# Performance work log

Hardware: AMD Instinct MI355X
Metric: run time of the kernel (lower is better)

The kernel has to match this reference:

```python
import jax, jax.numpy as jnp
import numpy as np

N = 8192
IN_DIM = 1024
HID = 64
N_CLASS = 40
N_LAYERS = 4  # N_LAYERS-1 hidden GraphConvolutions + 1 output layer


def _row_normalize(a):
    return a / jnp.clip(a.sum(axis=1, keepdims=True), 1e-6)


def setup_inputs() -> dict:
    key = jax.random.key(0)
    ks = jax.random.split(key, 10)
    x = jax.random.normal(ks[0], (N, IN_DIM), dtype=jnp.float32)
    # symmetric-ish normalized dense adjacency surrogates
    adj1 = _row_normalize(jax.random.uniform(ks[1], (N, N), dtype=jnp.float32))
    adj2 = _row_normalize(jax.random.uniform(ks[2], (N, N), dtype=jnp.float32))
    s_in = 1.0 / np.sqrt(IN_DIM)
    s_h = 1.0 / np.sqrt(HID)
    fc1_W = jax.random.uniform(ks[3], (IN_DIM, HID), minval=-s_in, maxval=s_in)
    fc1_b = jnp.zeros((HID,), jnp.float32)
    W_h = jax.random.uniform(ks[4], (N_LAYERS - 1, HID, HID), minval=-s_h, maxval=s_h)
    b_h = jnp.zeros((N_LAYERS - 1, HID), jnp.float32)
    W_out = jax.random.uniform(ks[5], (HID, N_CLASS), minval=-s_h, maxval=s_h)
    b_out = jnp.zeros((N_CLASS,), jnp.float32)
    return {"x": x, "adj1": adj1, "adj2": adj2, "fc1_W": fc1_W, "fc1_b": fc1_b,
            "W_h": W_h, "b_h": b_h, "W_out": W_out, "b_out": b_out}


def reference(x, adj1, adj2, fc1_W, fc1_b, W_h, b_h, W_out, b_out):
    # fc1 projection (dropout is identity in eval mode)
    h = x @ fc1_W + fc1_b  # [N, HID]
    # hidden GraphConvolution layers: aggregate, bias, residual, relu
    for i in range(W_h.shape[0]):
        h = jax.nn.relu(adj1 @ (h @ W_h[i]) + b_h[i] + h)
    # final layer: no residual
    out = jax.nn.relu(adj1 @ (h @ W_out) + b_out)  # [N, N_CLASS]
    return out
```

## Files before the change

kernel.cpp:

```cpp
#include <hip/hip_runtime.h>
#include <hip/hip_bf16.h>

typedef __attribute__((ext_vector_type(8))) short short8;
typedef __attribute__((ext_vector_type(4))) float f32x4;
typedef __attribute__((ext_vector_type(4))) int i32x4;

#define NROWS 8192
#define MTILE 128
#define SK 8
#define SA 400000.0f
#define SB 15.875f
#define INVQ (1.0f / (SA * SB))

__device__ inline short f2bf(float f) {
  union { float f; unsigned u; } v; v.f = f;
  unsigned r = v.u + 0x7FFFu + ((v.u >> 16) & 1u);
  return (short)(r >> 16);
}

__global__ __launch_bounds__(256) void prep_kernel(
    const float* __restrict__ x, const float* __restrict__ Wfc,
    float* __restrict__ P,
    const float* __restrict__ adj, char* __restrict__ AQ) {
  int bid = blockIdx.x;
  if (!AQ || bid < 1024) {
    __shared__ short Ws[64][136];
    int tid = threadIdx.x;
    int mb = bid & 127, yb = bid >> 7;
    int k0 = yb * 128;
    for (int i = tid; i < 2048; i += 256) {
      int k = i >> 4, nq = (i & 15) << 2;
      f32x4 v = *(const f32x4*)(Wfc + (size_t)(k0 + k) * 64 + nq);
      Ws[nq][k] = f2bf(v.x); Ws[nq + 1][k] = f2bf(v.y);
      Ws[nq + 2][k] = f2bf(v.z); Ws[nq + 3][k] = f2bf(v.w);
    }
    __syncthreads();
    int w = tid >> 6;
    int l = tid & 63;
    int l15 = l & 15, kg = l >> 4;
    int m_base = mb * 64 + w * 16;
    const float* Arow = x + (size_t)(m_base + l15) * 1024 + k0;
    f32x4 acc[4] = {{0,0,0,0},{0,0,0,0},{0,0,0,0},{0,0,0,0}};
#pragma unroll
    for (int k = 0; k < 128; k += 64) {
      f32x4 a32[2][2];
      short8 b[2][4];
#pragma unroll
      for (int u = 0; u < 2; ++u) {
        int kk = k + u * 32 + kg * 8;
        a32[u][0] = *(const f32x4*)(Arow + kk);
        a32[u][1] = *(const f32x4*)(Arow + kk + 4);
        b[u][0] = *(const short8*)&Ws[l15 +  0][kk];
        b[u][1] = *(const short8*)&Ws[l15 + 16][kk];
        b[u][2] = *(const short8*)&Ws[l15 + 32][kk];
        b[u][3] = *(const short8*)&Ws[l15 + 48][kk];
      }
#pragma unroll
      for (int u = 0; u < 2; ++u) {
        short8 af;
        af[0] = f2bf(a32[u][0].x); af[1] = f2bf(a32[u][0].y);
        af[2] = f2bf(a32[u][0].z); af[3] = f2bf(a32[u][0].w);
        af[4] = f2bf(a32[u][1].x); af[5] = f2bf(a32[u][1].y);
        af[6] = f2bf(a32[u][1].z); af[7] = f2bf(a32[u][1].w);
#pragma unroll
        for (int t = 0; t < 4; ++t)
          acc[t] = __builtin_amdgcn_mfma_f32_16x16x32_bf16(af, b[u][t], acc[t], 0, 0, 0);
      }
    }
    float* Pb = P + (size_t)yb * (NROWS * 64);
    int mr = m_base + kg * 4;
#pragma unroll
    for (int r = 0; r < 4; ++r) {
      size_t base = (size_t)(mr + r) * 64 + l15;
#pragma unroll
      for (int t = 0; t < 4; ++t) Pb[base + 16 * t] = acc[t][r];
    }
  } else {
    const size_t total = (size_t)NROWS * NROWS;
    size_t i0 = ((size_t)(bid - 1024) * 256 + threadIdx.x) * 16;
    size_t stride = (size_t)2048 * 256 * 16;
    for (size_t i = i0; i < total; i += stride) {
      i32x4 o;
#pragma unroll
      for (int q = 0; q < 4; ++q) {
        f32x4 v = __builtin_nontemporal_load((const f32x4*)(adj + i + 4 * q));
        int r0 = (int)(v.x * SA + 0.5f); r0 = r0 > 127 ? 127 : r0;
        int r1 = (int)(v.y * SA + 0.5f); r1 = r1 > 127 ? 127 : r1;
        int r2 = (int)(v.z * SA + 0.5f); r2 = r2 > 127 ? 127 : r2;
        int r3 = (int)(v.w * SA + 0.5f); r3 = r3 > 127 ? 127 : r3;
        o[q] = (r0 & 255) | ((r1 & 255) << 8) | ((r2 & 255) << 16) | ((r3 & 255) << 24);
      }
      *(i32x4*)(AQ + i) = o;
    }
  }
}

__global__ __launch_bounds__(256, 2) void gemm_i8_kernel(
    const char* __restrict__ AQ, const char* __restrict__ BQ,
    int* __restrict__ P) {
  __shared__ __align__(16) char Bs[64][1024 + 16];
  int tid = threadIdx.x;
  int w = tid >> 6, l = tid & 63;
  int l15 = l & 15, kg = l >> 4;
  int wrow = blockIdx.x * MTILE + w * 32;
  const int KCH = NROWS / SK;
  int k0 = blockIdx.y * KCH;
  const char* A0 = AQ + (size_t)(wrow + l15) * NROWS + k0;
  const char* A1 = AQ + (size_t)(wrow + 16 + l15) * NROWS + k0;

#pragma unroll
  for (int j = 0; j < 16; ++j) {
    int slot = tid + 256 * j;
    int r = slot >> 6, c = (slot & 63) << 4;
    i32x4 v = *(const i32x4*)(BQ + (size_t)r * NROWS + k0 + c);
    *(i32x4*)&Bs[r][c] = v;
  }
  __syncthreads();

  i32x4 acc[2][4];
#pragma unroll
  for (int rt = 0; rt < 2; ++rt)
#pragma unroll
    for (int ct = 0; ct < 4; ++ct) acc[rt][ct] = (i32x4){0, 0, 0, 0};

#pragma unroll 4
  for (int k = 0; k < KCH; k += 64) {
    int kk = k + kg * 16;
    i32x4 a0 = *(const i32x4*)(A0 + kk);
    i32x4 a1 = *(const i32x4*)(A1 + kk);
    i32x4 b0 = *(const i32x4*)&Bs[l15 +  0][kk];
    i32x4 b1 = *(const i32x4*)&Bs[l15 + 16][kk];
    i32x4 b2 = *(const i32x4*)&Bs[l15 + 32][kk];
    i32x4 b3 = *(const i32x4*)&Bs[l15 + 48][kk];
    acc[0][0] = __builtin_amdgcn_mfma_i32_16x16x64_i8(a0, b0, acc[0][0], 0, 0, 0);
    acc[0][1] = __builtin_amdgcn_mfma_i32_16x16x64_i8(a0, b1, acc[0][1], 0, 0, 0);
    acc[0][2] = __builtin_amdgcn_mfma_i32_16x16x64_i8(a0, b2, acc[0][2], 0, 0, 0);
    acc[0][3] = __builtin_amdgcn_mfma_i32_16x16x64_i8(a0, b3, acc[0][3], 0, 0, 0);
    acc[1][0] = __builtin_amdgcn_mfma_i32_16x16x64_i8(a1, b0, acc[1][0], 0, 0, 0);
    acc[1][1] = __builtin_amdgcn_mfma_i32_16x16x64_i8(a1, b1, acc[1][1], 0, 0, 0);
    acc[1][2] = __builtin_amdgcn_mfma_i32_16x16x64_i8(a1, b2, acc[1][2], 0, 0, 0);
    acc[1][3] = __builtin_amdgcn_mfma_i32_16x16x64_i8(a1, b3, acc[1][3], 0, 0, 0);
  }

  int* Pb = P + (size_t)blockIdx.y * (NROWS * 64);
#pragma unroll
  for (int rt = 0; rt < 2; ++rt)
#pragma unroll
    for (int r = 0; r < 4; ++r) {
      size_t base = (size_t)(wrow + rt * 16 + kg * 4 + r) * 64 + l15;
#pragma unroll
      for (int ct = 0; ct < 4; ++ct) Pb[base + 16 * ct] = acc[rt][ct][r];
    }
}

__global__ __launch_bounds__(256) void fused_rs_kernel(
    const float* __restrict__ Pf, const int* __restrict__ Pi,
    const float* __restrict__ bias, const float* __restrict__ Hres,
    const float* __restrict__ Wmat, int Nout,
    float* __restrict__ Hout, char* __restrict__ tQ, short* __restrict__ tB,
    int useint, int dores, int wantq) {
  __shared__ float hs[64][68];
  __shared__ float Ws[64][64];
  int tid = threadIdx.x;
  for (int i = tid; i < 64 * 64; i += 256) {
    int j = i >> 6, n = i & 63;
    Ws[j][n] = (n < Nout) ? Wmat[j * Nout + n] : 0.0f;
  }
  int r = tid >> 2;
  int c0 = (tid & 3) << 4;
  size_t gbase = ((size_t)blockIdx.x * 64 + r) * 64 + c0;
  f32x4 s[4] = {{0,0,0,0},{0,0,0,0},{0,0,0,0},{0,0,0,0}};
  if (useint) {
    i32x4 si[4] = {{0,0,0,0},{0,0,0,0},{0,0,0,0},{0,0,0,0}};
    for (int sidx = 0; sidx < SK; ++sidx) {
      const int* Pp = Pi + (size_t)sidx * ((size_t)NROWS * 64) + gbase;
#pragma unroll
      for (int q = 0; q < 4; ++q) si[q] += *(const i32x4*)(Pp + 4 * q);
    }
#pragma unroll
    for (int q = 0; q < 4; ++q) s[q] = __builtin_convertvector(si[q], f32x4) * INVQ;
  } else {
    for (int sidx = 0; sidx < SK; ++sidx) {
      const float* Pp = Pf + (size_t)sidx * ((size_t)NROWS * 64) + gbase;
#pragma unroll
      for (int q = 0; q < 4; ++q) s[q] += *(const f32x4*)(Pp + 4 * q);
    }
  }
#pragma unroll
  for (int q = 0; q < 4; ++q) {
    f32x4 v = s[q] + *(const f32x4*)(bias + c0 + 4 * q);
    if (dores) {
      v += *(const f32x4*)(Hres + gbase + 4 * q);
      v.x = v.x > 0.f ? v.x : 0.f; v.y = v.y > 0.f ? v.y : 0.f;
      v.z = v.z > 0.f ? v.z : 0.f; v.w = v.w > 0.f ? v.w : 0.f;
    }
    *(f32x4*)(Hout + gbase + 4 * q) = v;
    *(f32x4*)&hs[r][c0 + 4 * q] = v;
  }
  __syncthreads();
  int m = tid >> 2;
  int nq = (tid & 3) << 4;
  float hr[64];
#pragma unroll
  for (int j = 0; j < 64; j += 4) {
    f32x4 v = *(const f32x4*)&hs[m][j];
    hr[j] = v.x; hr[j + 1] = v.y; hr[j + 2] = v.z; hr[j + 3] = v.w;
  }
  size_t mglob = (size_t)blockIdx.x * 64 + m;
#pragma unroll
  for (int ni = 0; ni < 16; ++ni) {
    int n = nq + ni;
    float acc = 0.0f;
#pragma unroll
    for (int j = 0; j < 64; ++j) acc += hr[j] * Ws[j][n];
    if (wantq) {
      int q = __float2int_rn(acc * SB);
      q = q > 127 ? 127 : (q < -127 ? -127 : q);
      tQ[(size_t)n * NROWS + mglob] = (char)q;
    } else {
      tB[(size_t)n * NROWS + mglob] = f2bf(acc);
    }
  }
}

__global__ __launch_bounds__(256, 2) void gemm_a32_u2(
    const float* __restrict__ A, const short* __restrict__ BT,
    float* __restrict__ P, int K) {
  int w = threadIdx.x >> 6;
  int l = threadIdx.x & 63;
  int l15 = l & 15, kg = l >> 4;
  int m_base = blockIdx.x * 64 + w * 16;
  const float* Arow = A + (size_t)(m_base + l15) * K;
  const short* Br = BT + (size_t)l15 * K;
  int kchunk = K / SK;
  int k0 = blockIdx.y * kchunk;
  f32x4 acc[4] = {{0,0,0,0},{0,0,0,0},{0,0,0,0},{0,0,0,0}};
  for (int k = k0; k < k0 + kchunk; k += 64) {
    f32x4 a32[2][2];
    short8 b[2][4];
#pragma unroll
    for (int u = 0; u < 2; ++u) {
      int kk = k + u * 32 + kg * 8;
      a32[u][0] = __builtin_nontemporal_load((const f32x4*)(Arow + kk));
      a32[u][1] = __builtin_nontemporal_load((const f32x4*)(Arow + kk + 4));
      b[u][0] = *(const short8*)(Br + kk);
      b[u][1] = *(const short8*)(Br + (size_t)16 * K + kk);
      b[u][2] = *(const short8*)(Br + (size_t)32 * K + kk);
      b[u][3] = *(const short8*)(Br + (size_t)48 * K + kk);
    }
#pragma unroll
    for (int u = 0; u < 2; ++u) {
      short8 af;
      af[0] = f2bf(a32[u][0].x); af[1] = f2bf(a32[u][0].y);
      af[2] = f2bf(a32[u][0].z); af[3] = f2bf(a32[u][0].w);
      af[4] = f2bf(a32[u][1].x); af[5] = f2bf(a32[u][1].y);
      af[6] = f2bf(a32[u][1].z); af[7] = f2bf(a32[u][1].w);
#pragma unroll
      for (int t = 0; t < 4; ++t)
        acc[t] = __builtin_amdgcn_mfma_f32_16x16x32_bf16(af, b[u][t], acc[t], 0, 0, 0);
    }
  }
  float* Pb = P + (size_t)blockIdx.y * (NROWS * 64);
  int mr = m_base + kg * 4;
#pragma unroll
  for (int r = 0; r < 4; ++r) {
    size_t base = (size_t)(mr + r) * 64 + l15;
#pragma unroll
    for (int t = 0; t < 4; ++t) Pb[base + 16 * t] = acc[t][r];
  }
}

__global__ __launch_bounds__(256) void reduce_out_kernel(
    const float* __restrict__ Pf, const int* __restrict__ Pi,
    const float* __restrict__ bias, float* __restrict__ Out, int useint) {
  int gid = blockIdx.x * 256 + threadIdx.x;
  int e0 = gid * 4;
  int n = e0 & 63;
  if (n >= 40) return;
  f32x4 s = {0, 0, 0, 0};
  if (useint) {
    i32x4 si = {0, 0, 0, 0};
    for (int sidx = 0; sidx < SK; ++sidx)
      si += *(const i32x4*)(Pi + (size_t)sidx * (NROWS * 64) + e0);
    s = __builtin_convertvector(si, f32x4) * INVQ;
  } else {
    for (int sidx = 0; sidx < SK; ++sidx)
      s += *(const f32x4*)(Pf + (size_t)sidx * (NROWS * 64) + e0);
  }
  s += *(const f32x4*)(bias + n);
  s.x = s.x > 0.f ? s.x : 0.f; s.y = s.y > 0.f ? s.y : 0.f;
  s.z = s.z > 0.f ? s.z : 0.f; s.w = s.w > 0.f ? s.w : 0.f;
  int m = e0 >> 6;
  *(f32x4*)(Out + (size_t)m * 40 + n) = s;
}

extern "C" void kernel_launch(void* const* d_in, const int* in_sizes, int n_in,
                              void* d_out, int out_size, void* d_ws, size_t ws_size,
                              hipStream_t stream) {
  const float* x     = (const float*)d_in[0];
  const float* adj1  = (const float*)d_in[1];
  const float* fc1_W = (const float*)d_in[3];
  const float* fc1_b = (const float*)d_in[4];
  const float* W_h   = (const float*)d_in[5];
  const float* b_h   = (const float*)d_in[6];
  const float* W_out = (const float*)d_in[7];
  const float* b_out = (const float*)d_in[8];
  float* out = (float*)d_out;

  char* ws = (char*)d_ws;
  size_t off = 0;
  float* P    = (float*)(ws + off); off += (size_t)SK * NROWS * 64 * 4;
  int*   Pi   = (int*)P;
  float* h_a  = (float*)(ws + off); off += (size_t)NROWS * 64 * 4;
  float* h_b  = (float*)(ws + off); off += (size_t)NROWS * 64 * 4;
  short* tB   = (short*)(ws + off); off += (size_t)64 * NROWS * 2;
  char*  tQ   = (char*)(ws + off);  off += (size_t)64 * NROWS;
  size_t aq_bytes = (size_t)NROWS * NROWS;
  char*  AQ   = (ws_size - off >= aq_bytes) ? (char*)(ws + off) : nullptr;
  int ok = AQ != nullptr;

  prep_kernel<<<ok ? 3072 : 1024, 256, 0, stream>>>(x, fc1_W, P, adj1, AQ);

  fused_rs_kernel<<<NROWS / 64, 256, 0, stream>>>(
      P, nullptr, fc1_b, nullptr, W_h, 64, h_a, tQ, tB, 0, 0, ok);

  float* hc = h_a; float* hn = h_b;
  for (int i = 0; i < 3; ++i) {
    if (ok)
      gemm_i8_kernel<<<dim3(NROWS / MTILE, SK), 256, 0, stream>>>(AQ, tQ, Pi);
    else
      gemm_a32_u2<<<dim3(NROWS / 64, SK), 256, 0, stream>>>(adj1, tB, P, NROWS);
    const float* Wn = (i < 2) ? (W_h + (size_t)(i + 1) * 64 * 64) : W_out;
    int Nn = (i < 2) ? 64 : 40;
    fused_rs_kernel<<<NROWS / 64, 256, 0, stream>>>(
        P, Pi, b_h + (size_t)i * 64, hc, Wn, Nn, hn, tQ, tB, ok, 1, ok);
    float* t = hc; hc = hn; hn = t;
  }

  if (ok)
    gemm_i8_kernel<<<dim3(NROWS / MTILE, SK), 256, 0, stream>>>(AQ, tQ, Pi);
  else
    gemm_a32_u2<<<dim3(NROWS / 64, SK), 256, 0, stream>>>(adj1, tB, P, NROWS);
  reduce_out_kernel<<<NROWS * 64 / 4 / 256, 256, 0, stream>>>(P, Pi, b_out, out, ok);
}
```

Before: 233.5 us.

## Fuse split-K reduction and next-layer projection into GEMM via last-block atomic counter

Each split-K GEMM block now bumps a per-row-tile atomic counter after writing its partials. The last block to finish reduces all partials, applies bias, residual and relu, and computes the next layer's projection into a ping-ponged int8 buffer. This removes the separate fused_rs and reduce_out kernel launches and their dependent round trips. In exchange it adds threadfences, an atomic and a memset, and the reduction runs serially in only one of the SK blocks per tile, which may leave the tail of the grid underused.

```diff
diff --git a/kernel.cpp b/kernel.cpp
--- a/kernel.cpp
+++ b/kernel.cpp
@@ -18,14 +18,23 @@
   return (short)(r >> 16);
 }
 
+__device__ inline float relu4x(float a) { return a > 0.f ? a : 0.f; }
+
 __global__ __launch_bounds__(256) void prep_kernel(
     const float* __restrict__ x, const float* __restrict__ Wfc,
-    float* __restrict__ P,
+    const float* __restrict__ fc1_b, const float* __restrict__ W0,
+    float* __restrict__ P, float* __restrict__ h0,
+    char* __restrict__ tQ, short* __restrict__ tB, int wantq,
+    unsigned* __restrict__ cnt,
     const float* __restrict__ adj, char* __restrict__ AQ) {
   int bid = blockIdx.x;
+  int tid = threadIdx.x;
   if (!AQ || bid < 1024) {
-    __shared__ short Ws[64][136];
-    int tid = threadIdx.x;
+    __shared__ __align__(16) char smem[17408 + 16384];
+    short (*Ws)[136] = (short(*)[136])smem;
+    float (*hs)[68]  = (float(*)[68])smem;
+    float (*Wf)[64]  = (float(*)[64])(smem + 17408);
+    __shared__ unsigned isred;
     int mb = bid & 127, yb = bid >> 7;
     int k0 = yb * 128;
     for (int i = tid; i < 2048; i += 256) {
@@ -35,8 +44,7 @@
       Ws[nq + 2][k] = f2bf(v.z); Ws[nq + 3][k] = f2bf(v.w);
     }
     __syncthreads();
-    int w = tid >> 6;
-    int l = tid & 63;
+    int w = tid >> 6, l = tid & 63;
     int l15 = l & 15, kg = l >> 4;
     int m_base = mb * 64 + w * 16;
     const float* Arow = x + (size_t)(m_base + l15) * 1024 + k0;
@@ -67,7 +75,7 @@
           acc[t] = __builtin_amdgcn_mfma_f32_16x16x32_bf16(af, b[u][t], acc[t], 0, 0, 0);
       }
     }
-    float* Pb = P + (size_t)yb * (NROWS * 64);
+    float* Pb = P + (size_t)yb * ((size_t)NROWS * 64);
     int mr = m_base + kg * 4;
 #pragma unroll
     for (int r = 0; r < 4; ++r) {
@@ -75,9 +83,53 @@
 #pragma unroll
       for (int t = 0; t < 4; ++t) Pb[base + 16 * t] = acc[t][r];
     }
+    __threadfence();
+    __syncthreads();
+    if (tid == 0) isred = (atomicAdd(&cnt[mb], 1u) == SK - 1) ? 1u : 0u;
+    __syncthreads();
+    if (!isred) return;
+    __threadfence();
+    for (int i = tid; i < 4096; i += 256) Wf[i >> 6][i & 63] = W0[i];
+    int r = tid >> 2, c0 = (tid & 3) << 4;
+    size_t gbase = ((size_t)mb * 64 + r) * 64 + c0;
+    f32x4 s[4] = {{0,0,0,0},{0,0,0,0},{0,0,0,0},{0,0,0,0}};
+    for (int sidx = 0; sidx < SK; ++sidx) {
+      const float* Pp = P + (size_t)sidx * ((size_t)NROWS * 64) + gbase;
+#pragma unroll
+      for (int q = 0; q < 4; ++q) s[q] += *(const f32x4*)(Pp + 4 * q);
+    }
+#pragma unroll
+    for (int q = 0; q < 4; ++q) {
+      f32x4 v = s[q] + *(const f32x4*)(fc1_b + c0 + 4 * q);
+      *(f32x4*)(h0 + gbase + 4 * q) = v;
+      *(f32x4*)&hs[r][c0 + 4 * q] = v;
+    }
+    __syncthreads();
+    int m = tid >> 2, nq = (tid & 3) << 4;
+    float hr[64];
+#pragma unroll
+    for (int j = 0; j < 64; j += 4) {
+      f32x4 v = *(const f32x4*)&hs[m][j];
+      hr[j] = v.x; hr[j + 1] = v.y; hr[j + 2] = v.z; hr[j + 3] = v.w;
+    }
+    size_t mglob = (size_t)mb * 64 + m;
+#pragma unroll
+    for (int ni = 0; ni < 16; ++ni) {
+      int n = nq + ni;
+      float a2 = 0.f;
+#pragma unroll
+      for (int j = 0; j < 64; ++j) a2 += hr[j] * Wf[j][n];
+      if (wantq) {
+        int q = __float2int_rn(a2 * SB);
+        q = q > 127 ? 127 : (q < -127 ? -127 : q);
+        tQ[(size_t)n * NROWS + mglob] = (char)q;
+      } else {
+        tB[(size_t)n * NROWS + mglob] = f2bf(a2);
+      }
+    }
   } else {
     const size_t total = (size_t)NROWS * NROWS;
-    size_t i0 = ((size_t)(bid - 1024) * 256 + threadIdx.x) * 16;
+    size_t i0 = ((size_t)(bid - 1024) * 256 + tid) * 16;
     size_t stride = (size_t)2048 * 256 * 16;
     for (size_t i = i0; i < total; i += stride) {
       i32x4 o;
@@ -95,14 +147,20 @@
   }
 }
 
-__global__ __launch_bounds__(256, 2) void gemm_i8_kernel(
+__global__ __launch_bounds__(256, 2) void gemm_i8f_kernel(
     const char* __restrict__ AQ, const char* __restrict__ BQ,
-    int* __restrict__ P) {
+    int* __restrict__ P, unsigned* __restrict__ cnt,
+    const float* __restrict__ bias, const float* __restrict__ Hres,
+    const float* __restrict__ Wnext, int Nout,
+    float* __restrict__ Hout, char* __restrict__ tQn,
+    float* __restrict__ Out, int mode) {
   __shared__ __align__(16) char Bs[64][1024 + 16];
+  __shared__ unsigned isred;
   int tid = threadIdx.x;
   int w = tid >> 6, l = tid & 63;
   int l15 = l & 15, kg = l >> 4;
-  int wrow = blockIdx.x * MTILE + w * 32;
+  int mb = blockIdx.x;
+  int wrow = mb * MTILE + w * 32;
   const int KCH = NROWS / SK;
   int k0 = blockIdx.y * KCH;
   const char* A0 = AQ + (size_t)(wrow + l15) * NROWS + k0;
@@ -112,8 +170,7 @@
   for (int j = 0; j < 16; ++j) {
     int slot = tid + 256 * j;
     int r = slot >> 6, c = (slot & 63) << 4;
-    i32x4 v = *(const i32x4*)(BQ + (size_t)r * NROWS + k0 + c);
-    *(i32x4*)&Bs[r][c] = v;
+    *(i32x4*)&Bs[r][c] = *(const i32x4*)(BQ + (size_t)r * NROWS + k0 + c);
   }
   __syncthreads();
 
@@ -142,7 +199,7 @@
     acc[1][3] = __builtin_amdgcn_mfma_i32_16x16x64_i8(a1, b3, acc[1][3], 0, 0, 0);
   }
 
-  int* Pb = P + (size_t)blockIdx.y * (NROWS * 64);
+  int* Pb = P + (size_t)blockIdx.y * ((size_t)NROWS * 64);
 #pragma unroll
   for (int rt = 0; rt < 2; ++rt)
 #pragma unroll
@@ -151,75 +208,71 @@
 #pragma unroll
       for (int ct = 0; ct < 4; ++ct) Pb[base + 16 * ct] = acc[rt][ct][r];
     }
-}
-
-__global__ __launch_bounds__(256) void fused_rs_kernel(
-    const float* __restrict__ Pf, const int* __restrict__ Pi,
-    const float* __restrict__ bias, const float* __restrict__ Hres,
-    const float* __restrict__ Wmat, int Nout,
-    float* __restrict__ Hout, char* __restrict__ tQ, short* __restrict__ tB,
-    int useint, int dores, int wantq) {
-  __shared__ float hs[64][68];
-  __shared__ float Ws[64][64];
-  int tid = threadIdx.x;
-  for (int i = tid; i < 64 * 64; i += 256) {
-    int j = i >> 6, n = i & 63;
-    Ws[j][n] = (n < Nout) ? Wmat[j * Nout + n] : 0.0f;
-  }
-  int r = tid >> 2;
-  int c0 = (tid & 3) << 4;
-  size_t gbase = ((size_t)blockIdx.x * 64 + r) * 64 + c0;
-  f32x4 s[4] = {{0,0,0,0},{0,0,0,0},{0,0,0,0},{0,0,0,0}};
-  if (useint) {
+
+  __threadfence();
+  __syncthreads();
+  if (tid == 0) isred = (atomicAdd(&cnt[mb], 1u) == SK - 1) ? 1u : 0u;
+  __syncthreads();
+  if (!isred) return;
+  __threadfence();
+
+  float (*hs)[68] = (float(*)[68])&Bs[0][0];
+  float (*Wf)[64] = (float(*)[64])((char*)&Bs[0][0] + 17408);
+  if (mode == 0) {
+    for (int i = tid; i < 4096; i += 256) {
+      int j = i >> 6, n = i & 63;
+      Wf[j][n] = (n < Nout) ? Wnext[j * Nout + n] : 0.0f;
+    }
+  }
+  for (int half = 0; half < 2; ++half) {
+    int row0 = mb * MTILE + half * 64;
+    int r = tid >> 2, c0 = (tid & 3) << 4;
+    size_t gbase = ((size_t)row0 + r) * 64 + c0;
     i32x4 si[4] = {{0,0,0,0},{0,0,0,0},{0,0,0,0},{0,0,0,0}};
     for (int sidx = 0; sidx < SK; ++sidx) {
-      const int* Pp = Pi + (size_t)sidx * ((size_t)NROWS * 64) + gbase;
+      const int* Pp = P + (size_t)sidx * ((size_t)NROWS * 64) + gbase;
 #pragma unroll
       for (int q = 0; q < 4; ++q) si[q] += *(const i32x4*)(Pp + 4 * q);
     }
 #pragma unroll
-    for (int q = 0; q < 4; ++q) s[q] = __builtin_convertvector(si[q], f32x4) * INVQ;
-  } else {
-    for (int sidx = 0; sidx < SK; ++sidx) {
-      const float* Pp = Pf + (size_t)sidx * ((size_t)NROWS * 64) + gbase;
-#pragma unroll
-      for (int q = 0; q < 4; ++q) s[q] += *(const f32x4*)(Pp + 4 * q);
-    }
-  }
-#pragma unroll
-  for (int q = 0; q < 4; ++q) {
-    f32x4 v = s[q] + *(const f32x4*)(bias + c0 + 4 * q);
-    if (dores) {
-      v += *(const f32x4*)(Hres + gbase + 4 * q);
-      v.x = v.x > 0.f ? v.x : 0.f; v.y = v.y > 0.f ? v.y : 0.f;
-      v.z = v.z > 0.f ? v.z : 0.f; v.w = v.w > 0.f ? v.w : 0.f;
-    }
-    *(f32x4*)(Hout + gbase + 4 * q) = v;
-    *(f32x4*)&hs[r][c0 + 4 * q] = v;
-  }
-  __syncthreads();
-  int m = tid >> 2;
-  int nq = (tid & 3) << 4;
-  float hr[64];
-#pragma unroll
-  for (int j = 0; j < 64; j += 4) {
-    f32x4 v = *(const f32x4*)&hs[m][j];
-    hr[j] = v.x; hr[j + 1] = v.y; hr[j + 2] = v.z; hr[j + 3] = v.w;
-  }
-  size_t mglob = (size_t)blockIdx.x * 64 + m;
-#pragma unroll
-  for (int ni = 0; ni < 16; ++ni) {
-    int n = nq + ni;
-    float acc = 0.0f;
-#pragma unroll
-    for (int j = 0; j < 64; ++j) acc += hr[j] * Ws[j][n];
-    if (wantq) {
-      int q = __float2int_rn(acc * SB);
-      q = q > 127 ? 127 : (q < -127 ? -127 : q);
-      tQ[(size_t)n * NROWS + mglob] = (char)q;
-    } else {
-      tB[(size_t)n * NROWS + mglob] = f2bf(acc);
-    }
+    for (int q = 0; q < 4; ++q) {
+      f32x4 v = __builtin_convertvector(si[q], f32x4) * INVQ;
+      v += *(const f32x4*)(bias + c0 + 4 * q);
+      if (mode == 0) {
+        v += *(const f32x4*)(Hres + gbase + 4 * q);
+        v.x = relu4x(v.x); v.y = relu4x(v.y); v.z = relu4x(v.z); v.w = relu4x(v.w);
+        *(f32x4*)(Hout + gbase + 4 * q) = v;
+        *(f32x4*)&hs[r][c0 + 4 * q] = v;
+      } else {
+#pragma unroll
+        for (int e = 0; e < 4; ++e) {
+          int n = c0 + 4 * q + e;
+          if (n < 40) Out[((size_t)row0 + r) * 40 + n] = relu4x(v[e]);
+        }
+      }
+    }
+    __syncthreads();
+    if (mode == 0) {
+      int m = tid >> 2, nq = (tid & 3) << 4;
+      float hr[64];
+#pragma unroll
+      for (int j = 0; j < 64; j += 4) {
+        f32x4 v = *(const f32x4*)&hs[m][j];
+        hr[j] = v.x; hr[j + 1] = v.y; hr[j + 2] = v.z; hr[j + 3] = v.w;
+      }
+      size_t mglob = (size_t)row0 + m;
+#pragma unroll
+      for (int ni = 0; ni < 16; ++ni) {
+        int n = nq + ni;
+        float a2 = 0.f;
+#pragma unroll
+        for (int j = 0; j < 64; ++j) a2 += hr[j] * Wf[j][n];
+        int q = __float2int_rn(a2 * SB);
+        q = q > 127 ? 127 : (q < -127 ? -127 : q);
+        tQn[(size_t)n * NROWS + mglob] = (char)q;
+      }
+    }
+    __syncthreads();
   }
 }
 
@@ -270,26 +323,69 @@
   }
 }
 
+__global__ __launch_bounds__(256) void fused_rs_kernel(
+    const float* __restrict__ Pf,
+    const float* __restrict__ bias, const float* __restrict__ Hres,
+    const float* __restrict__ Wmat, int Nout,
+    float* __restrict__ Hout, short* __restrict__ tB, int dores) {
+  __shared__ float hs[64][68];
+  __shared__ float Ws[64][64];
+  int tid = threadIdx.x;
+  for (int i = tid; i < 64 * 64; i += 256) {
+    int j = i >> 6, n = i & 63;
+    Ws[j][n] = (n < Nout) ? Wmat[j * Nout + n] : 0.0f;
+  }
+  int r = tid >> 2;
+  int c0 = (tid & 3) << 4;
+  size_t gbase = ((size_t)blockIdx.x * 64 + r) * 64 + c0;
+  f32x4 s[4] = {{0,0,0,0},{0,0,0,0},{0,0,0,0},{0,0,0,0}};
+  for (int sidx = 0; sidx < SK; ++sidx) {
+    const float* Pp = Pf + (size_t)sidx * ((size_t)NROWS * 64) + gbase;
+#pragma unroll
+    for (int q = 0; q < 4; ++q) s[q] += *(const f32x4*)(Pp + 4 * q);
+  }
+#pragma unroll
+  for (int q = 0; q < 4; ++q) {
+    f32x4 v = s[q] + *(const f32x4*)(bias + c0 + 4 * q);
+    if (dores) {
+      v += *(const f32x4*)(Hres + gbase + 4 * q);
+      v.x = relu4x(v.x); v.y = relu4x(v.y); v.z = relu4x(v.z); v.w = relu4x(v.w);
+    }
+    *(f32x4*)(Hout + gbase + 4 * q) = v;
+    *(f32x4*)&hs[r][c0 + 4 * q] = v;
+  }
+  __syncthreads();
+  int m = tid >> 2;
+  int nq = (tid & 3) << 4;
+  float hr[64];
+#pragma unroll
+  for (int j = 0; j < 64; j += 4) {
+    f32x4 v = *(const f32x4*)&hs[m][j];
+    hr[j] = v.x; hr[j + 1] = v.y; hr[j + 2] = v.z; hr[j + 3] = v.w;
+  }
+  size_t mglob = (size_t)blockIdx.x * 64 + m;
+#pragma unroll
+  for (int ni = 0; ni < 16; ++ni) {
+    int n = nq + ni;
+    float a2 = 0.0f;
+#pragma unroll
+    for (int j = 0; j < 64; ++j) a2 += hr[j] * Ws[j][n];
+    tB[(size_t)n * NROWS + mglob] = f2bf(a2);
+  }
+}
+
 __global__ __launch_bounds__(256) void reduce_out_kernel(
-    const float* __restrict__ Pf, const int* __restrict__ Pi,
-    const float* __restrict__ bias, float* __restrict__ Out, int useint) {
+    const float* __restrict__ Pf, const float* __restrict__ bias,
+    float* __restrict__ Out) {
   int gid = blockIdx.x * 256 + threadIdx.x;
   int e0 = gid * 4;
   int n = e0 & 63;
   if (n >= 40) return;
   f32x4 s = {0, 0, 0, 0};
-  if (useint) {
-    i32x4 si = {0, 0, 0, 0};
-    for (int sidx = 0; sidx < SK; ++sidx)
-      si += *(const i32x4*)(Pi + (size_t)sidx * (NROWS * 64) + e0);
-    s = __builtin_convertvector(si, f32x4) * INVQ;
-  } else {
-    for (int sidx = 0; sidx < SK; ++sidx)
-      s += *(const f32x4*)(Pf + (size_t)sidx * (NROWS * 64) + e0);
-  }
+  for (int sidx = 0; sidx < SK; ++sidx)
+    s += *(const f32x4*)(Pf + (size_t)sidx * (NROWS * 64) + e0);
   s += *(const f32x4*)(bias + n);
-  s.x = s.x > 0.f ? s.x : 0.f; s.y = s.y > 0.f ? s.y : 0.f;
-  s.z = s.z > 0.f ? s.z : 0.f; s.w = s.w > 0.f ? s.w : 0.f;
+  s.x = relu4x(s.x); s.y = relu4x(s.y); s.z = relu4x(s.z); s.w = relu4x(s.w);
   int m = e0 >> 6;
   *(f32x4*)(Out + (size_t)m * 40 + n) = s;
 }
@@ -313,33 +409,45 @@
   int*   Pi   = (int*)P;
   float* h_a  = (float*)(ws + off); off += (size_t)NROWS * 64 * 4;
   float* h_b  = (float*)(ws + off); off += (size_t)NROWS * 64 * 4;
+  char*  tQa  = (char*)(ws + off);  off += (size_t)64 * NROWS;
+  char*  tQb  = (char*)(ws + off);  off += (size_t)64 * NROWS;
   short* tB   = (short*)(ws + off); off += (size_t)64 * NROWS * 2;
-  char*  tQ   = (char*)(ws + off);  off += (size_t)64 * NROWS;
+  unsigned* cnt = (unsigned*)(ws + off); off += 4096;
   size_t aq_bytes = (size_t)NROWS * NROWS;
   char*  AQ   = (ws_size - off >= aq_bytes) ? (char*)(ws + off) : nullptr;
   int ok = AQ != nullptr;
 
-  prep_kernel<<<ok ? 3072 : 1024, 256, 0, stream>>>(x, fc1_W, P, adj1, AQ);
-
-  fused_rs_kernel<<<NROWS / 64, 256, 0, stream>>>(
-      P, nullptr, fc1_b, nullptr, W_h, 64, h_a, tQ, tB, 0, 0, ok);
-
-  float* hc = h_a; float* hn = h_b;
-  for (int i = 0; i < 3; ++i) {
-    if (ok)
-      gemm_i8_kernel<<<dim3(NROWS / MTILE, SK), 256, 0, stream>>>(AQ, tQ, Pi);
-    else
+  hipMemsetAsync(cnt, 0, 4096, stream);
+
+  prep_kernel<<<ok ? 3072 : 1024, 256, 0, stream>>>(
+      x, fc1_W, fc1_b, W_h, P, h_a, tQa, tB, ok, cnt, adj1, AQ);
+
+  if (ok) {
+    float* hc = h_a; float* hn = h_b;
+    char* tin = tQa; char* tout = tQb;
+    for (int i = 0; i < 3; ++i) {
+      const float* Wn = (i < 2) ? (W_h + (size_t)(i + 1) * 64 * 64) : W_out;
+      int Nn = (i < 2) ? 64 : 40;
+      gemm_i8f_kernel<<<dim3(64, SK), 256, 0, stream>>>(
+          AQ, tin, Pi, cnt + 128 + i * 64, b_h + (size_t)i * 64, hc, Wn, Nn,
+          hn, tout, nullptr, 0);
+      float* t = hc; hc = hn; hn = t;
+      char* tq = tin; tin = tout; tout = tq;
+    }
+    gemm_i8f_kernel<<<dim3(64, SK), 256, 0, stream>>>(
+        AQ, tin, Pi, cnt + 128 + 3 * 64, b_out, nullptr, nullptr, 0,
+        nullptr, nullptr, out, 1);
+  } else {
+    float* hc = h_a; float* hn = h_b;
+    for (int i = 0; i < 3; ++i) {
       gemm_a32_u2<<<dim3(NROWS / 64, SK), 256, 0, stream>>>(adj1, tB, P, NROWS);
-    const float* Wn = (i < 2) ? (W_h + (size_t)(i + 1) * 64 * 64) : W_out;
-    int Nn = (i < 2) ? 64 : 40;
-    fused_rs_kernel<<<NROWS / 64, 256, 0, stream>>>(
-        P, Pi, b_h + (size_t)i * 64, hc, Wn, Nn, hn, tQ, tB, ok, 1, ok);
-    float* t = hc; hc = hn; hn = t;
-  }
-
-  if (ok)
-    gemm_i8_kernel<<<dim3(NROWS / MTILE, SK), 256, 0, stream>>>(AQ, tQ, Pi);
-  else
+      const float* Wn = (i < 2) ? (W_h + (size_t)(i + 1) * 64 * 64) : W_out;
+      int Nn = (i < 2) ? 64 : 40;
+      fused_rs_kernel<<<NROWS / 64, 256, 0, stream>>>(
+          P, b_h + (size_t)i * 64, hc, Wn, Nn, hn, tB, 1);
+      float* t = hc; hc = hn; hn = t;
+    }
     gemm_a32_u2<<<dim3(NROWS / 64, SK), 256, 0, stream>>>(adj1, tB, P, NROWS);
-  reduce_out_kernel<<<NROWS * 64 / 4 / 256, 256, 0, stream>>>(P, Pi, b_out, out, ok);
-}
+    reduce_out_kernel<<<NROWS * 64 / 4 / 256, 256, 0, stream>>>(P, b_out, out);
+  }
+}
```

Result: slower. 701.7 us (+200.5%).
